# Kernel tuning notes

Measured on AMD Instinct MI355X. Metric: run time of the kernel, lower is better.

## Reference

```python
import jax, jax.numpy as jnp
import numpy as np


def setup_inputs() -> dict:
    key = jax.random.key(0)
    k1, k2 = jax.random.split(key)
    pred = jax.random.normal(k1, (4, 8192, 3), dtype=jnp.float32)
    label = jax.random.normal(k2, (4, 8192, 3), dtype=jnp.float32)
    return {"pred": pred, "label": label}


def reference(pred, label):
    # Pairwise Euclidean distances via the Gram-matrix identity
    # explicit repeat+subtract+norm, without the [B,N,M,D] blowup).
    x2 = jnp.sum(pred * pred, axis=-1)            # [B, N]
    y2 = jnp.sum(label * label, axis=-1)          # [B, M]
    xy = jnp.einsum('bnd,bmd->bnm', pred, label)  # [B, N, M]
    d2 = x2[:, :, None] + y2[:, None, :] - 2.0 * xy
    dis = jnp.sqrt(jnp.maximum(d2, 0.0))          # [B, N, M]
    dis_xy = jnp.mean(jnp.min(dis, axis=2))       # pred -> nearest label
    dis_yx = jnp.mean(jnp.min(dis, axis=1))       # label -> nearest pred
    return dis_xy + dis_yx
```

## Files before the change

kernel.cpp:

```cpp
#include <hip/hip_runtime.h>
#include <math.h>

#define BATCH 4
#define NPTS 8192
#define TPB 256
#define RPT 4
#define ROWS_PER_BLOCK (TPB * RPT)
#define ROW_TILES (NPTS / ROWS_PER_BLOCK)

__global__ __launch_bounds__(TPB) void chamfer_partial(
    const float* __restrict__ pred, const float* __restrict__ label,
    float* __restrict__ ws, int S, int colsPerSeg) {
  const int tid = threadIdx.x;
  const int seg = blockIdx.x % S;
  const int rowTile = blockIdx.x / S;
  const int b = blockIdx.y;
  const int dir = blockIdx.z;
  const float* __restrict__ rows = (dir == 0) ? pred : label;
  const float* __restrict__ cols = (dir == 0) ? label : pred;

  float x0[RPT], x1[RPT], x2[RPT], x2n[RPT], mn[RPT];
  const int rowBase = rowTile * ROWS_PER_BLOCK;
#pragma unroll
  for (int r = 0; r < RPT; ++r) {
    const int row = rowBase + r * TPB + tid;
    const float* p = rows + ((size_t)b * NPTS + row) * 3;
    x0[r] = p[0];
    x1[r] = p[1];
    x2[r] = p[2];
    x2n[r] = x0[r] * x0[r] + x1[r] * x1[r] + x2[r] * x2[r];
    mn[r] = INFINITY;
  }

  __shared__ float4 sh[TPB];
  const int colBase = seg * colsPerSeg;
  for (int c0 = 0; c0 < colsPerSeg; c0 += TPB) {
    __syncthreads();
    {
      const int col = colBase + c0 + tid;
      const float* q = cols + ((size_t)b * NPTS + col) * 3;
      const float y0 = q[0], y1 = q[1], y2 = q[2];
      sh[tid] = make_float4(-2.0f * y0, -2.0f * y1, -2.0f * y2,
                            y0 * y0 + y1 * y1 + y2 * y2);
    }
    __syncthreads();
#pragma unroll 4
    for (int l = 0; l < TPB; l += 2) {
      const float4 ya = sh[l];
      const float4 yb = sh[l + 1];
#pragma unroll
      for (int r = 0; r < RPT; ++r) {
        float ta = fmaf(x0[r], ya.x, ya.w);
        ta = fmaf(x1[r], ya.y, ta);
        ta = fmaf(x2[r], ya.z, ta);
        float tb = fmaf(x0[r], yb.x, yb.w);
        tb = fmaf(x1[r], yb.y, tb);
        tb = fmaf(x2[r], yb.z, tb);
        mn[r] = fminf(mn[r], fminf(ta, tb));
      }
    }
  }

#pragma unroll
  for (int r = 0; r < RPT; ++r) {
    const int row = rowBase + r * TPB + tid;
    ws[(((size_t)dir * BATCH + b) * S + seg) * NPTS + row] = x2n[r] + mn[r];
  }
}

__global__ __launch_bounds__(256) void chamfer_reduce(
    const float* __restrict__ ws, float* __restrict__ out, int S) {
  const int g0 = blockIdx.x * 1024 + threadIdx.x;
  float sum = 0.0f;
#pragma unroll
  for (int k = 0; k < 4; ++k) {
    const int g = g0 + k * 256;
    const int db = g / NPTS;
    const int row = g & (NPTS - 1);
    const float* p = ws + (size_t)db * S * NPTS + row;
    float m = p[0];
    for (int s = 1; s < S; ++s) m = fminf(m, p[(size_t)s * NPTS]);
    m = fmaxf(m, 0.0f);
    sum += sqrtf(m);
  }
  sum *= (1.0f / (float)(BATCH * NPTS));
  for (int off = 32; off > 0; off >>= 1) sum += __shfl_down(sum, off, 64);
  __shared__ float ssum[4];
  const int wid = threadIdx.x >> 6;
  const int lane = threadIdx.x & 63;
  if (lane == 0) ssum[wid] = sum;
  __syncthreads();
  if (threadIdx.x == 0) atomicAdd(out, ssum[0] + ssum[1] + ssum[2] + ssum[3]);
}

extern "C" void kernel_launch(void* const* d_in, const int* in_sizes, int n_in,
                              void* d_out, int out_size, void* d_ws,
                              size_t ws_size, hipStream_t stream) {
  const float* pred = (const float*)d_in[0];
  const float* label = (const float*)d_in[1];
  float* out = (float*)d_out;
  float* ws = (float*)d_ws;

  int S = 16;
  while (S > 1 && (size_t)2 * BATCH * S * NPTS * sizeof(float) > ws_size)
    S >>= 1;
  const int colsPerSeg = NPTS / S;

  hipMemsetAsync(d_out, 0, sizeof(float), stream);

  dim3 grid1(ROW_TILES * S, BATCH, 2);
  chamfer_partial<<<grid1, TPB, 0, stream>>>(pred, label, ws, S, colsPerSeg);
  chamfer_reduce<<<64, 256, 0, stream>>>(ws, out, S);
}
```

Measured before the change: 116.3 us.

## Use packed FP32 FMA with 16 rows per thread and 32 column segments

Each thread now handles 16 rows instead of 4. The inner loop uses inline v_pk_fma_f32 to score two rows per instruction and v_min3_f32 to fold the minima. Column data sits in SoA shared memory, loaded once per block for a 256-column segment split 32 ways. The memset is dropped in favour of zeroing the output inside the partial kernel, and the reduce kernel now uses one thread per row. This aims to cut VALU instruction count and host/launch overhead, at the cost of higher register pressure and no workspace-size fallback.

```diff
diff --git a/kernel.cpp b/kernel.cpp
--- a/kernel.cpp
+++ b/kernel.cpp
@@ -4,91 +4,152 @@
 #define BATCH 4
 #define NPTS 8192
 #define TPB 256
-#define RPT 4
+#define RPT 16
 #define ROWS_PER_BLOCK (TPB * RPT)
 #define ROW_TILES (NPTS / ROWS_PER_BLOCK)
+#define SEGS 32
+#define COLS_PER_SEG (NPTS / SEGS)
+#define NGROUPS (2 * BATCH * ROW_TILES)
 
-__global__ __launch_bounds__(TPB) void chamfer_partial(
+typedef float v2f __attribute__((ext_vector_type(2)));
+typedef float v4f __attribute__((ext_vector_type(4)));
+
+#define PK_NEW_L(t, xp, y, c)                                        \
+  asm("v_pk_fma_f32 %0, %1, %2, %3 op_sel:[0,0,0] op_sel_hi:[0,1,1]" \
+      : "=v"(t) : "v"(xp), "v"(y), "v"(c))
+#define PK_ACC_L(t, xp, y)                                           \
+  asm("v_pk_fma_f32 %0, %1, %2, %0 op_sel:[0,0,0] op_sel_hi:[0,1,1]" \
+      : "+v"(t) : "v"(xp), "v"(y))
+#define PK_NEW_H(t, xp, y, c)                                        \
+  asm("v_pk_fma_f32 %0, %1, %2, %3 op_sel:[1,0,0] op_sel_hi:[1,1,1]" \
+      : "=v"(t) : "v"(xp), "v"(y), "v"(c))
+#define PK_ACC_H(t, xp, y)                                           \
+  asm("v_pk_fma_f32 %0, %1, %2, %0 op_sel:[1,0,0] op_sel_hi:[1,1,1]" \
+      : "+v"(t) : "v"(xp), "v"(y))
+#define MIN3(mn, ta, tb) \
+  asm("v_min3_f32 %0, %0, %1, %2" : "+v"(mn) : "v"(ta), "v"(tb))
+
+#define ROWPAIR(i, y0, y1, y2, yq)   \
+  do {                               \
+    v2f tA, tB;                      \
+    PK_NEW_L(tA, xp##i##0, y0, yq);  \
+    PK_ACC_L(tA, xp##i##1, y1);      \
+    PK_ACC_L(tA, xp##i##2, y2);      \
+    float tal = tA.x, tah = tA.y;    \
+    MIN3(mnA##i, tal, tah);          \
+    PK_NEW_H(tB, xp##i##0, y0, yq);  \
+    PK_ACC_H(tB, xp##i##1, y1);      \
+    PK_ACC_H(tB, xp##i##2, y2);      \
+    float tbl = tB.x, tbh = tB.y;    \
+    MIN3(mnB##i, tbl, tbh);          \
+  } while (0)
+
+#define LOADX2(i)                                                              \
+  const float* pA##i =                                                         \
+      rows + ((size_t)(rowGlobal + (2 * (i)) * TPB + tid)) * 3;                \
+  const float* pB##i =                                                         \
+      rows + ((size_t)(rowGlobal + (2 * (i) + 1) * TPB + tid)) * 3;            \
+  const float aA##i##0 = pA##i[0], aA##i##1 = pA##i[1], aA##i##2 = pA##i[2];   \
+  const float aB##i##0 = pB##i[0], aB##i##1 = pB##i[1], aB##i##2 = pB##i[2];   \
+  const v2f xp##i##0 = {aA##i##0, aB##i##0};                                   \
+  const v2f xp##i##1 = {aA##i##1, aB##i##1};                                   \
+  const v2f xp##i##2 = {aA##i##2, aB##i##2};                                   \
+  const float nA##i =                                                          \
+      aA##i##0 * aA##i##0 + aA##i##1 * aA##i##1 + aA##i##2 * aA##i##2;         \
+  const float nB##i =                                                          \
+      aB##i##0 * aB##i##0 + aB##i##1 * aB##i##1 + aB##i##2 * aB##i##2;         \
+  float mnA##i = INFINITY, mnB##i = INFINITY;
+
+__global__ __launch_bounds__(TPB, 2) void chamfer_partial(
     const float* __restrict__ pred, const float* __restrict__ label,
-    float* __restrict__ ws, int S, int colsPerSeg) {
+    float* __restrict__ ws, float* __restrict__ out) {
   const int tid = threadIdx.x;
-  const int seg = blockIdx.x % S;
-  const int rowTile = blockIdx.x / S;
+  const int seg = blockIdx.x & (SEGS - 1);
+  const int rowTile = blockIdx.x >> 5;
   const int b = blockIdx.y;
   const int dir = blockIdx.z;
+  const int g = (dir * BATCH + b) * ROW_TILES + rowTile;
   const float* __restrict__ rows = (dir == 0) ? pred : label;
   const float* __restrict__ cols = (dir == 0) ? label : pred;
 
-  float x0[RPT], x1[RPT], x2[RPT], x2n[RPT], mn[RPT];
-  const int rowBase = rowTile * ROWS_PER_BLOCK;
-#pragma unroll
-  for (int r = 0; r < RPT; ++r) {
-    const int row = rowBase + r * TPB + tid;
-    const float* p = rows + ((size_t)b * NPTS + row) * 3;
-    x0[r] = p[0];
-    x1[r] = p[1];
-    x2[r] = p[2];
-    x2n[r] = x0[r] * x0[r] + x1[r] * x1[r] + x2[r] * x2[r];
-    mn[r] = INFINITY;
+  if (blockIdx.x == 0 && b == 0 && dir == 0 && tid == 0) out[0] = 0.0f;
+
+  __shared__ __align__(16) float sm0[COLS_PER_SEG];
+  __shared__ __align__(16) float sm1[COLS_PER_SEG];
+  __shared__ __align__(16) float sm2[COLS_PER_SEG];
+  __shared__ __align__(16) float sq[COLS_PER_SEG];
+
+  {
+    const float* q =
+        cols + ((size_t)(b * NPTS + seg * COLS_PER_SEG + tid)) * 3;
+    const float y0 = q[0], y1 = q[1], y2 = q[2];
+    sm0[tid] = -2.0f * y0;
+    sm1[tid] = -2.0f * y1;
+    sm2[tid] = -2.0f * y2;
+    sq[tid] = y0 * y0 + y1 * y1 + y2 * y2;
   }
 
-  __shared__ float4 sh[TPB];
-  const int colBase = seg * colsPerSeg;
-  for (int c0 = 0; c0 < colsPerSeg; c0 += TPB) {
-    __syncthreads();
+  const int rowGlobal = b * NPTS + rowTile * ROWS_PER_BLOCK;
+  LOADX2(0) LOADX2(1) LOADX2(2) LOADX2(3)
+  LOADX2(4) LOADX2(5) LOADX2(6) LOADX2(7)
+
+  __syncthreads();
+
+#pragma unroll 2
+  for (int l = 0; l < COLS_PER_SEG; l += 4) {
+    const v4f a0 = *(const v4f*)&sm0[l];
+    const v4f a1 = *(const v4f*)&sm1[l];
+    const v4f a2 = *(const v4f*)&sm2[l];
+    const v4f a3 = *(const v4f*)&sq[l];
     {
-      const int col = colBase + c0 + tid;
-      const float* q = cols + ((size_t)b * NPTS + col) * 3;
-      const float y0 = q[0], y1 = q[1], y2 = q[2];
-      sh[tid] = make_float4(-2.0f * y0, -2.0f * y1, -2.0f * y2,
-                            y0 * y0 + y1 * y1 + y2 * y2);
+      const v2f y0 = a0.lo, y1 = a1.lo, y2 = a2.lo, yq = a3.lo;
+      ROWPAIR(0, y0, y1, y2, yq);
+      ROWPAIR(1, y0, y1, y2, yq);
+      ROWPAIR(2, y0, y1, y2, yq);
+      ROWPAIR(3, y0, y1, y2, yq);
+      ROWPAIR(4, y0, y1, y2, yq);
+      ROWPAIR(5, y0, y1, y2, yq);
+      ROWPAIR(6, y0, y1, y2, yq);
+      ROWPAIR(7, y0, y1, y2, yq);
     }
-    __syncthreads();
-#pragma unroll 4
-    for (int l = 0; l < TPB; l += 2) {
-      const float4 ya = sh[l];
-      const float4 yb = sh[l + 1];
-#pragma unroll
-      for (int r = 0; r < RPT; ++r) {
-        float ta = fmaf(x0[r], ya.x, ya.w);
-        ta = fmaf(x1[r], ya.y, ta);
-        ta = fmaf(x2[r], ya.z, ta);
-        float tb = fmaf(x0[r], yb.x, yb.w);
-        tb = fmaf(x1[r], yb.y, tb);
-        tb = fmaf(x2[r], yb.z, tb);
-        mn[r] = fminf(mn[r], fminf(ta, tb));
-      }
+    {
+      const v2f y0 = a0.hi, y1 = a1.hi, y2 = a2.hi, yq = a3.hi;
+      ROWPAIR(0, y0, y1, y2, yq);
+      ROWPAIR(1, y0, y1, y2, yq);
+      ROWPAIR(2, y0, y1, y2, yq);
+      ROWPAIR(3, y0, y1, y2, yq);
+      ROWPAIR(4, y0, y1, y2, yq);
+      ROWPAIR(5, y0, y1, y2, yq);
+      ROWPAIR(6, y0, y1, y2, yq);
+      ROWPAIR(7, y0, y1, y2, yq);
     }
   }
 
-#pragma unroll
-  for (int r = 0; r < RPT; ++r) {
-    const int row = rowBase + r * TPB + tid;
-    ws[(((size_t)dir * BATCH + b) * S + seg) * NPTS + row] = x2n[r] + mn[r];
-  }
+  float* wsl = ws + ((size_t)g * SEGS + seg) * ROWS_PER_BLOCK + tid;
+#define STORE2(i)                                   \
+  wsl[(2 * (i)) * TPB] = nA##i + mnA##i;            \
+  wsl[(2 * (i) + 1) * TPB] = nB##i + mnB##i;
+  STORE2(0) STORE2(1) STORE2(2) STORE2(3)
+  STORE2(4) STORE2(5) STORE2(6) STORE2(7)
+#undef STORE2
 }
 
 __global__ __launch_bounds__(256) void chamfer_reduce(
-    const float* __restrict__ ws, float* __restrict__ out, int S) {
-  const int g0 = blockIdx.x * 1024 + threadIdx.x;
-  float sum = 0.0f;
+    const float* __restrict__ ws, float* __restrict__ out) {
+  const int r = blockIdx.x * 256 + threadIdx.x;
+  const int db = r >> 13;
+  const int rowInB = r & (NPTS - 1);
+  const int rowTile = rowInB >> 12;
+  const int rloc = rowInB & (ROWS_PER_BLOCK - 1);
+  const int g = db * ROW_TILES + rowTile;
+  const float* p = ws + (size_t)g * SEGS * ROWS_PER_BLOCK + rloc;
+  float m = INFINITY;
 #pragma unroll
-  for (int k = 0; k < 4; ++k) {
-    const int g = g0 + k * 256;
-    const int db = g / NPTS;
-    const int row = g & (NPTS - 1);
-    const float* p = ws + (size_t)db * S * NPTS + row;
-    float m = p[0];
-    for (int s = 1; s < S; ++s) m = fminf(m, p[(size_t)s * NPTS]);
-    m = fmaxf(m, 0.0f);
-    sum += sqrtf(m);
-  }
-  sum *= (1.0f / (float)(BATCH * NPTS));
+  for (int s = 0; s < SEGS; ++s) m = fminf(m, p[(size_t)s * ROWS_PER_BLOCK]);
+  float sum = sqrtf(fmaxf(m, 0.0f)) * (1.0f / (float)(BATCH * NPTS));
   for (int off = 32; off > 0; off >>= 1) sum += __shfl_down(sum, off, 64);
   __shared__ float ssum[4];
-  const int wid = threadIdx.x >> 6;
-  const int lane = threadIdx.x & 63;
-  if (lane == 0) ssum[wid] = sum;
+  if ((threadIdx.x & 63) == 0) ssum[threadIdx.x >> 6] = sum;
   __syncthreads();
   if (threadIdx.x == 0) atomicAdd(out, ssum[0] + ssum[1] + ssum[2] + ssum[3]);
 }
@@ -100,15 +161,7 @@
   const float* label = (const float*)d_in[1];
   float* out = (float*)d_out;
   float* ws = (float*)d_ws;
-
-  int S = 16;
-  while (S > 1 && (size_t)2 * BATCH * S * NPTS * sizeof(float) > ws_size)
-    S >>= 1;
-  const int colsPerSeg = NPTS / S;
-
-  hipMemsetAsync(d_out, 0, sizeof(float), stream);
-
-  dim3 grid1(ROW_TILES * S, BATCH, 2);
-  chamfer_partial<<<grid1, TPB, 0, stream>>>(pred, label, ws, S, colsPerSeg);
-  chamfer_reduce<<<64, 256, 0, stream>>>(ws, out, S);
+  dim3 grid1(ROW_TILES * SEGS, BATCH, 2);
+  chamfer_partial<<<grid1, TPB, 0, stream>>>(pred, label, ws, out);
+  chamfer_reduce<<<NPTS * 2 * BATCH / 256, 256, 0, stream>>>(ws, out);
 }
```

Measured after the change: 101.7 us. 12.6% less time.
